# Performance work log

Hardware: AMD Instinct MI355X
Metric: run time of the kernel (lower is better)

The kernel has to match this reference:

```python
import jax, jax.numpy as jnp
import numpy as np
jax.config.update("jax_enable_x64", True)

MS_H = 10
MS_W = 10
EPS = 1e-8


def _window_mean(x, kh, kw):
    # x: [B, H, W]; VALID avg-pool with kernel (kh, kw), stride 1, via integral image
    c = jnp.cumsum(jnp.cumsum(x, axis=1), axis=2)
    c = jnp.pad(c, ((0, 0), (1, 0), (1, 0)))
    H, W = x.shape[1], x.shape[2]
    oh, ow = H - kh + 1, W - kw + 1
    s = (c[:, kh:kh + oh, kw:kw + ow] - c[:, :oh, kw:kw + ow]
         - c[:, kh:kh + oh, :ow] + c[:, :oh, :ow])
    return s / (kh * kw)


def _translate_bilinear(imgs, dy, dx):
    # imgs: [B, H, W]; out[b,i,j] = imgs[b, i - dy[b], j - dx[b]] (bilinear, zero fill)
    B, H, W = imgs.shape
    yq = jnp.arange(H, dtype=imgs.dtype)[None, :, None] - dy[:, None, None]
    xq = jnp.arange(W, dtype=imgs.dtype)[None, None, :] - dx[:, None, None]
    y0 = jnp.floor(yq); x0 = jnp.floor(xq)
    wy = yq - y0;       wx = xq - x0
    y0i = y0.astype(jnp.int32); x0i = x0.astype(jnp.int32)
    b = jnp.arange(B)[:, None, None]
    def samp(yi, xi):
        valid = (yi >= 0) & (yi < H) & (xi >= 0) & (xi < W)
        v = imgs[b, jnp.clip(yi, 0, H - 1), jnp.clip(xi, 0, W - 1)]
        return jnp.where(valid, v, jnp.zeros((), imgs.dtype))
    v00 = samp(y0i, x0i);     v01 = samp(y0i, x0i + 1)
    v10 = samp(y0i + 1, x0i); v11 = samp(y0i + 1, x0i + 1)
    return (v00 * (1 - wy) * (1 - wx) + v01 * (1 - wy) * wx
            + v10 * wy * (1 - wx) + v11 * wy * wx)


def _motion_correct(fr, template):
    # fr: [1, B, H, W, 1] float32; template: [H, W] float32
    B = fr.shape[1]
    H, W = template.shape
    mx, my = H // 2, W // 2
    # --- template normalization ---
    t_zm = template - jnp.mean(template)
    t_var = jnp.sum(jnp.square(t_zm)) + EPS
    target_freq = jnp.fft.fft2(t_zm.astype(jnp.complex128))            # [H, W]
    imgs = fr[0, :, :, :, 0]                                           # [B, H, W]
    imgs_zm = imgs - jnp.mean(imgs, axis=(1, 2), keepdims=True)
    # --- local statistics (avg_pool2d VALID, kernel = template minus shift margins) ---
    kh, kw = H - 2 * MS_W, W - 2 * MS_H
    m1 = _window_mean(imgs, kh, kw)                                    # [B, 2mw+1, 2mh+1]
    m2 = _window_mean(jnp.square(imgs), kh, kw)
    imgs_var = m2 - jnp.square(m1) / (kh * kw) + EPS
    imgs_var = jnp.where(imgs_var < 0, 0.0, imgs_var)
    denominator = jnp.sqrt(t_var * imgs_var)
    # --- FFT cross-correlation (fft3d over batch+spatial, exactly as the TF code) ---
    fr_freq = jnp.fft.fftn(imgs_zm.astype(jnp.complex128), axes=(0, 1, 2))
    img_product = fr_freq * jnp.conj(target_freq)[None]
    cc = jnp.abs(jnp.fft.ifftn(img_product, axes=(0, 1, 2))).astype(jnp.float32)
    rolled = jnp.roll(cc, (B, mx, my), axis=(0, 1, 2))
    nom = rolled[:, mx - MS_W:mx + MS_W + 1, my - MS_H:my + MS_H + 1]
    ncc = nom / denominator
    ncc = jnp.where(jnp.isnan(ncc), 0.0, ncc)                          # [B, 2mw+1, 2mh+1]
    # --- integer peak ---
    flat = ncc.reshape(B, -1)
    am = jnp.argmax(flat, axis=1)
    shx = am // (2 * MS_H + 1)
    shy = am % (2 * MS_H + 1)
    sh_x_n = -(shx - MS_H).astype(jnp.float32)
    sh_y_n = -(shy - MS_W).astype(jnp.float32)
    # --- log-parabolic sub-pixel refinement ---
    l = jnp.log(ncc)
    b = jnp.arange(B)
    lxm1 = l[b, shx - 1, shy]; lxp1 = l[b, shx + 1, shy]
    lym1 = l[b, shx, shy - 1]; lyp1 = l[b, shx, shy + 1]
    lc4 = 4.0 * l[b, shx, shy]
    sh_x_n = sh_x_n - (lxm1 - lxp1) / (2 * lxm1 - lc4 + 2 * lxp1)
    sh_y_n = sh_y_n - (lym1 - lyp1) / (2 * lym1 - lc4 + 2 * lyp1)
    # --- bilinear translate; tfa translations = [sh_y (dx, width), sh_x (dy, height)] ---
    warped = _translate_bilinear(imgs, sh_x_n, sh_y_n)                 # [B, H, W]
    return jnp.transpose(warped, (0, 2, 1)).reshape(B, H * W)


def setup_inputs() -> dict:
    H = W = 512
    B = 32
    k1, k2, k3 = jax.random.split(jax.random.key(0), 3)
    # smooth (low-pass) random template so the NCC peak is smooth/positive around its max
    noise = jax.random.normal(k1, (H, W))
    f = jnp.sqrt(jnp.fft.fftfreq(H)[:, None] ** 2 + jnp.fft.fftfreq(W)[None, :] ** 2)
    lp = (f < 0.05).astype(jnp.complex128)
    template = jnp.real(jnp.fft.ifft2(jnp.fft.fft2(noise) * lp))
    template = (template / template.std()).astype(jnp.float32)
    # frames: template shifted by small random integer offsets + noise
    shifts = jax.random.randint(k2, (B, 2), -5, 6)
    frames = jax.vmap(lambda s: jnp.roll(template, (s[0], s[1]), axis=(0, 1)))(shifts)
    frames = frames + 0.05 * jax.random.normal(k3, (B, H, W), dtype=jnp.float32)
    fr = frames[None, :, :, :, None].astype(jnp.float32)
    return {"fr": fr, "template": template}


def reference(fr, template):
    return _motion_correct(fr, template)
```

## Files before the change

kernel.cpp:

```cpp
#include <hip/hip_runtime.h>
#include <math.h>

#define HH 512
#define WW 512
#define NPIX (HH*WW)
#define NB 32
#define NS 21
#define KWIN 492
#define NKB 256
#define MT28 28
#define PARTSZ (MT28*32*16)
#define TPLB_COPY 278528

typedef __attribute__((ext_vector_type(8))) short short8;
typedef __attribute__((ext_vector_type(4))) float floatx4;

__device__ __forceinline__ unsigned short f2bf(float f) {
    unsigned u = __float_as_uint(f);
    unsigned r = (u + 0x7fffu + ((u >> 16) & 1u)) >> 16;
    return (unsigned short)r;
}

__device__ __forceinline__ short8 loadA(const unsigned short* p) {
    union { short8 v; unsigned u[4]; } r;
    const unsigned* q = (const unsigned*)p;
    r.u[0] = q[0]; r.u[1] = q[1]; r.u[2] = q[2]; r.u[3] = q[3];
    return r.v;
}

__global__ __launch_bounds__(512) void prep_tpl(
    const float* __restrict__ tpl, unsigned short* __restrict__ tplb)
{
    int t   = threadIdx.x;
    int sy0 = blockIdx.x * 4;
#pragma unroll
    for (int rr = 0; rr < 4; ++rr) {
        int sy = sy0 + rr;
        const float* srow = tpl + (size_t)sy * WW;
#pragma unroll
        for (int P = 0; P < 2; ++P) {
            for (int c = t; c < 544; c += 512) {
                int sx = (c + 496 - P) & 511;
                tplb[(size_t)P * TPLB_COPY + (size_t)sy * 544 + c] = f2bf(srow[sx]);
            }
        }
    }
}

__global__ __launch_bounds__(896) void corr_mfma(
    const float* __restrict__ fr, const unsigned short* __restrict__ tplb,
    const float* __restrict__ tpl, float* __restrict__ part,
    float* __restrict__ I1p, float* __restrict__ I2p,
    double* __restrict__ tplS1p, double* __restrict__ tplS2p)
{
    __shared__ unsigned short Bs[16384];
    __shared__ double jb1[8], jb2[8];

    const int blk = blockIdx.x;
    const int t   = threadIdx.x;

    if (blk >= 512) {
        int tj = blk - 512;
        if (t < 512) {
            const float* trow = tpl + (size_t)tj * 8 * WW;
            float s1 = 0.f, s2 = 0.f;
            for (int y = 0; y < 8; ++y) {
                float v = trow[(size_t)y * WW + t];
                s1 += v; s2 += v * v;
            }
            double d1 = (double)s1, d2 = (double)s2;
            for (int off = 32; off; off >>= 1) {
                d1 += __shfl_down(d1, off);
                d2 += __shfl_down(d2, off);
            }
            int lane = t & 63, wv = t >> 6;
            if (lane == 0) { jb1[wv] = d1; jb2[wv] = d2; }
        }
        __syncthreads();
        if (t == 0) {
            double a = 0.0, c = 0.0;
            for (int i = 0; i < 8; ++i) { a += jb1[i]; c += jb2[i]; }
            tplS1p[tj] = a; tplS2p[tj] = c;
        }
        return;
    }
    if (blk >= 256) {
        if (t < 512) {
            int id = blk - 256;
            int b = id >> 3, oct = id & 7;
            const float* img = fr + (size_t)b * NPIX;
            float s1 = 0.f, s2 = 0.f;
            int y0 = 20 + 59 * oct;
            for (int y = y0; y < y0 + 59; ++y) {
                float v = img[(size_t)y * WW + t];
                s1 += v; s2 += v * v;
            }
            I1p[(size_t)id * 512 + t] = s1;
            I2p[(size_t)id * 512 + t] = s2;
        }
        return;
    }

    const int l   = t & 63;
    const int wid = t >> 6;
    const int idx = blk;
    const int kb  = ((idx & 7) << 5) | (idx >> 3);
    const int kg  = l >> 4;
    const int ln  = l & 15;

    int du0, dv0, du1, dv1;
    {
        int m_g = 32 * wid + ln;
        du0 = (m_g * 1561) >> 15;
        dv0 = m_g - 21 * du0;
        if (m_g >= 441) { du0 = 0; dv0 = 0; }
        m_g = 32 * wid + 16 + ln;
        du1 = (m_g * 1561) >> 15;
        dv1 = m_g - 21 * du1;
        if (m_g >= 441) { du1 = 0; dv1 = 0; }
    }
    const int P0 = dv0 & 1, P1 = dv1 & 1;
    const int col0 = 8 * kg - dv0 + 26 + P0;
    const int col1 = 8 * kg - dv1 + 26 + P1;

    const unsigned short* lB = Bs + kg * 256 + ln * 8;

    floatx4 acc00 = {}, acc01 = {}, acc10 = {}, acc11 = {};

#pragma unroll 1
    for (int c = 0; c < 2; ++c) {
        const int row = 2 * kb + c;
        const int k0  = row << 9;
        if (c) __syncthreads();
        for (int i = t; i < 4096; i += 896) {
            int frame = i >> 7, q = i & 127;
            float4 v = *(const float4*)(fr + (size_t)frame * NPIX + k0 + 4 * q);
            int k8 = q >> 1, j4 = (q & 1) * 4;
            ushort4 o;
            o.x = f2bf(v.x); o.y = f2bf(v.y); o.z = f2bf(v.z); o.w = f2bf(v.w);
            *(ushort4*)&Bs[(k8 * 32 + frame) * 8 + j4] = o;
        }
        __syncthreads();

        const unsigned short* pA0 = tplb + (size_t)P0 * TPLB_COPY
            + (size_t)((row + 522 - du0) & 511) * 544 + col0;
        const unsigned short* pA1 = tplb + (size_t)P1 * TPLB_COPY
            + (size_t)((row + 522 - du1) & 511) * 544 + col1;

#pragma unroll
        for (int ks = 0; ks < 16; ++ks) {
            short8 A0 = loadA(pA0);
            short8 A1 = loadA(pA1);
            short8 B0 = *(const short8*)(lB + ks * 1024);
            short8 B1 = *(const short8*)(lB + ks * 1024 + 128);
            acc00 = __builtin_amdgcn_mfma_f32_16x16x32_bf16(A0, B0, acc00, 0, 0, 0);
            acc01 = __builtin_amdgcn_mfma_f32_16x16x32_bf16(A0, B1, acc01, 0, 0, 0);
            acc10 = __builtin_amdgcn_mfma_f32_16x16x32_bf16(A1, B0, acc10, 0, 0, 0);
            acc11 = __builtin_amdgcn_mfma_f32_16x16x32_bf16(A1, B1, acc11, 0, 0, 0);
            pA0 += 32; pA1 += 32;
        }
    }

    {
        size_t base = ((size_t)kb * MT28 + 2 * wid) * 32;
        floatx4* p;
        p = (floatx4*)(part + (base + ln)      * 16 + 4 * kg); *p = acc00;
        p = (floatx4*)(part + (base + 16 + ln) * 16 + 4 * kg); *p = acc01;
        p = (floatx4*)(part + (base + 32 + ln) * 16 + 4 * kg); *p = acc10;
        p = (floatx4*)(part + (base + 48 + ln) * 16 + 4 * kg); *p = acc11;
    }
}

__global__ __launch_bounds__(512) void reduce_k(
    const float* __restrict__ part, float* __restrict__ cc8)
{
    int blk = blockIdx.x;
    int oct = blk / 28;
    int j   = (blk % 28) * 512 + threadIdx.x;
    const float* p = part + (size_t)(oct * 32) * PARTSZ + j;
    float s = 0.f;
#pragma unroll 8
    for (int i = 0; i < 32; ++i)
        s += p[(size_t)i * PARTSZ];
    cc8[(size_t)oct * PARTSZ + j] = s;
}

__global__ __launch_bounds__(512) void stage2_am(
    const float* __restrict__ cc8, const float* __restrict__ fr,
    const float* __restrict__ I1p, const float* __restrict__ I2p,
    const double* __restrict__ tplS1p, const double* __restrict__ tplS2p,
    float* __restrict__ shifts)
{
    __shared__ double wr1[NS][8], wr2[NS][8], wrT[8];
    __shared__ float  e1[NS][40], e2[NS][40];
    __shared__ double totals1[NS], totals2[NS];
    __shared__ float  denomS[NS * NS];
    __shared__ double tS1s, tS2s, sum1b;

    int b = blockIdx.x;
    int x = threadIdx.x;
    const float* img = fr + (size_t)b * NPIX;
    float top[20], bot[20];
#pragma unroll
    for (int y = 0; y < 20; ++y) top[y] = img[(size_t)y * WW + x];
#pragma unroll
    for (int y = 0; y < 20; ++y) bot[y] = img[(size_t)(492 + y) * WW + x];

    float t1 = 0.f, t2 = 0.f, b1 = 0.f, b2 = 0.f;
#pragma unroll
    for (int y = 0; y < 20; ++y) {
        t1 += top[y]; t2 += top[y] * top[y];
        b1 += bot[y]; b2 += bot[y] * bot[y];
    }
    float i1 = 0.f, i2 = 0.f;
#pragma unroll
    for (int o = 0; o < 8; ++o) {
        i1 += I1p[((size_t)(b * 8 + o)) * 512 + x];
        i2 += I2p[((size_t)(b * 8 + o)) * 512 + x];
    }
    int lane = x & 63, wv = x >> 6;

    if (x < 64) {
        double d1 = tplS1p[x], d2 = tplS2p[x];
        for (int off = 32; off; off >>= 1) {
            d1 += __shfl_down(d1, off);
            d2 += __shfl_down(d2, off);
        }
        if (x == 0) { tS1s = d1; tS2s = d2; }
    }

    double tot = (double)i1 + (double)t1 + (double)b1;
    for (int off = 32; off; off >>= 1) tot += __shfl_down(tot, off);
    if (lane == 0) wrT[wv] = tot;

    float s1 = i1 + t1, s2 = i2 + t2;
#pragma unroll
    for (int u = 0; u < NS; ++u) {
        if (u) {
            float a = top[u-1], c = bot[u-1];
            s1 += c - a;
            s2 += c * c - a * a;
        }
        double d1 = (double)s1, d2 = (double)s2;
        for (int off = 32; off; off >>= 1) {
            d1 += __shfl_down(d1, off);
            d2 += __shfl_down(d2, off);
        }
        if (lane == 0) { wr1[u][wv] = d1; wr2[u][wv] = d2; }
        if (x < 20)        { e1[u][x]       = s1; e2[u][x]       = s2; }
        else if (x >= 492) { e1[u][x - 472] = s1; e2[u][x - 472] = s2; }
    }
    __syncthreads();
    if (x == 0) {
        double s = 0.0;
        for (int i = 0; i < 8; ++i) s += wrT[i];
        sum1b = s;
    }
    if (x < NS) {
        double a = 0.0, c = 0.0;
        for (int i = 0; i < 8; ++i) { a += wr1[x][i]; c += wr2[x][i]; }
        totals1[x] = a; totals2[x] = c;
    }
    __syncthreads();
    if (x < NS * NS) {
        int u = x / NS, v = x - NS * u;
        double S1 = totals1[u], S2 = totals2[u];
        for (int j = 0; j < v; ++j)  { S1 -= (double)e1[u][j];      S2 -= (double)e2[u][j]; }
        for (int j = v; j < 20; ++j) { S1 -= (double)e1[u][20 + j]; S2 -= (double)e2[u][20 + j]; }
        const double inv = 1.0 / ((double)KWIN * (double)KWIN);
        double m1 = S1 * inv, m2 = S2 * inv;
        double var = m2 - (m1 * m1) * inv + 1e-8;
        if (var < 0.0) var = 0.0;
        double tv = tS2s - tS1s * tS1s * (1.0 / (double)NPIX) + 1e-8;
        denomS[x] = (float)sqrt(tv * var);
    }
    __syncthreads();

    if (x < 64) {
        float corr = (float)(sum1b * tS1s * (1.0 / (double)NPIX));
        auto ccAt = [&](int m) -> float {
            int jj = ((m >> 4) * 512) + b * 16 + (m & 15);
            float s = 0.f;
#pragma unroll
            for (int o = 0; o < 8; ++o) s += cc8[(size_t)o * PARTSZ + jj];
            return s;
        };
        float best = -1e30f; int bidx = NS * NS;
        for (int i = x; i < NS * NS; i += 64) {
            float v = fabsf(ccAt(i) - corr) / denomS[i];
            if (v != v) v = 0.f;
            if (v > best) { best = v; bidx = i; }
        }
        for (int off = 32; off; off >>= 1) {
            float ov = __shfl_down(best, off);
            int   oi = __shfl_down(bidx, off);
            if (ov > best || (ov == best && oi < bidx)) { best = ov; bidx = oi; }
        }
        if (x == 0) {
            int shx = bidx / NS, shy = bidx % NS;
            auto nccAt = [&](int i, int j) -> float {
                i = (i < 0) ? i + NS : i; i = (i > NS - 1) ? NS - 1 : i;
                j = (j < 0) ? j + NS : j; j = (j > NS - 1) ? NS - 1 : j;
                float v = fabsf(ccAt(i * NS + j) - corr) / denomS[i * NS + j];
                if (v != v) v = 0.f;
                return v;
            };
            float lc  = logf(nccAt(shx, shy));
            float lxm = logf(nccAt(shx - 1, shy));
            float lxp = logf(nccAt(shx + 1, shy));
            float lym = logf(nccAt(shx, shy - 1));
            float lyp = logf(nccAt(shx, shy + 1));
            float shxn = -(float)(shx - 10) - (lxm - lxp) / (2.f * lxm - 4.f * lc + 2.f * lxp);
            float shyn = -(float)(shy - 10) - (lym - lyp) / (2.f * lym - 4.f * lc + 2.f * lyp);
            shifts[b]      = shxn;
            shifts[32 + b] = shyn;
        }
    }
}

__device__ __forceinline__ float samp(const float* __restrict__ img, int y, int x) {
    bool valid = (y >= 0) & (y < HH) & (x >= 0) & (x < WW);
    int yc = min(max(y, 0), HH - 1), xc = min(max(x, 0), WW - 1);
    float v = img[(size_t)yc * WW + xc];
    return valid ? v : 0.f;
}

__global__ __launch_bounds__(256) void warp_kernel(
    const float* __restrict__ fr, const float* __restrict__ shifts,
    float* __restrict__ out)
{
    int b  = blockIdx.z;
    int h0 = blockIdx.y * 32;
    int w0 = blockIdx.x * 32;
    float dy = shifts[b], dx = shifts[32 + b];
    const float* img = fr + (size_t)b * NPIX;
    __shared__ float tile[32][33];
    int tx = threadIdx.x & 31;
    int tz = threadIdx.x >> 5;
#pragma unroll
    for (int s = 0; s < 4; ++s) {
        int h = h0 + tz + 8 * s;
        int w = w0 + tx;
        float yq = (float)h - dy;
        float xq = (float)w - dx;
        float y0f = floorf(yq), x0f = floorf(xq);
        float wy = yq - y0f, wx = xq - x0f;
        int y0 = (int)y0f, x0 = (int)x0f;
        float v00 = samp(img, y0,     x0);
        float v01 = samp(img, y0,     x0 + 1);
        float v10 = samp(img, y0 + 1, x0);
        float v11 = samp(img, y0 + 1, x0 + 1);
        float val = v00 * (1.f - wy) * (1.f - wx) + v01 * (1.f - wy) * wx
                  + v10 * wy * (1.f - wx)         + v11 * wy * wx;
        tile[tz + 8 * s][tx] = val;
    }
    __syncthreads();
#pragma unroll
    for (int s = 0; s < 4; ++s) {
        int hh = tx;
        int ww = tz + 8 * s;
        out[(size_t)b * NPIX + (size_t)(w0 + ww) * HH + (h0 + hh)] = tile[hh][ww];
    }
}

extern "C" void kernel_launch(void* const* d_in, const int* in_sizes, int n_in,
                              void* d_out, int out_size, void* d_ws, size_t ws_size,
                              hipStream_t stream) {
    const float* fr  = (const float*)d_in[0];
    const float* tpl = (const float*)d_in[1];
    float* out = (float*)d_out;
    char* ws = (char*)d_ws;

    unsigned short* tplb = (unsigned short*)(ws + 0);
    float*  I1p    = (float*) (ws + 2097152);
    float*  I2p    = (float*) (ws + 2621440);
    double* tplS1p = (double*)(ws + 3145728);
    double* tplS2p = (double*)(ws + 3146240);
    float*  shifts = (float*) (ws + 3146752);
    float*  cc8    = (float*) (ws + 4194304);
    float*  part   = (float*) (ws + 8388608);

    prep_tpl  <<<128, 512, 0, stream>>>(tpl, tplb);
    corr_mfma <<<576, 896, 0, stream>>>(fr, tplb, tpl, part, I1p, I2p, tplS1p, tplS2p);
    reduce_k  <<<224, 512, 0, stream>>>(part, cc8);
    stage2_am <<<32, 512, 0, stream>>>(cc8, fr, I1p, I2p, tplS1p, tplS2p, shifts);
    warp_kernel<<<dim3(16, 16, 32), 256, 0, stream>>>(fr, shifts, out);
}
```

Baseline: 147.3 us.

## Precompute border row sums in corr kernel and simplify stage2 window totals

Adds 160 extra blocks to the correlation kernel that compute per-row double sums and sums of squares for the 20 top and 20 bottom rows of each frame. Stage2 then builds the 21 row-shift window totals with a serial prefix update instead of 21 block-wide shuffle reductions. Only the edge columns still load the bottom rows to fill the per-column edge tables. The intent is to shorten the serial, single-block-per-frame stage2 kernel. The cost is extra blocks in corr_mfma, and the window totals now mix double row sums with float column accumulations, which changes rounding slightly.

New measurement: 136.1 us. 1.08x faster.

```diff
diff --git a/kernel.cpp b/kernel.cpp
--- a/kernel.cpp
+++ b/kernel.cpp
@@ -51,7 +51,8 @@
     const float* __restrict__ fr, const unsigned short* __restrict__ tplb,
     const float* __restrict__ tpl, float* __restrict__ part,
     float* __restrict__ I1p, float* __restrict__ I2p,
-    double* __restrict__ tplS1p, double* __restrict__ tplS2p)
+    double* __restrict__ tplS1p, double* __restrict__ tplS2p,
+    double* __restrict__ rowS1, double* __restrict__ rowS2)
 {
     __shared__ unsigned short Bs[16384];
     __shared__ double jb1[8], jb2[8];
@@ -59,6 +60,29 @@
     const int blk = blockIdx.x;
     const int t   = threadIdx.x;
 
+    if (blk >= 576) {
+        int wvv = t >> 6;
+        if (wvv < 8) {
+            int rid  = (blk - 576) * 8 + wvv;
+            int lane = t & 63;
+            int b = rid / 40, j2 = rid % 40;
+            int y = (j2 < 20) ? j2 : (472 + j2);
+            const float* row = fr + (size_t)b * NPIX + (size_t)y * WW;
+            double d1 = 0.0, d2 = 0.0;
+#pragma unroll
+            for (int i = 0; i < 8; ++i) {
+                float v = row[lane + 64 * i];
+                d1 += (double)v;
+                d2 += (double)(v * v);
+            }
+            for (int off = 32; off; off >>= 1) {
+                d1 += __shfl_down(d1, off);
+                d2 += __shfl_down(d2, off);
+            }
+            if (lane == 0) { rowS1[rid] = d1; rowS2[rid] = d2; }
+        }
+        return;
+    }
     if (blk >= 512) {
         int tj = blk - 512;
         if (t < 512) {
@@ -189,29 +213,27 @@
     const float* __restrict__ cc8, const float* __restrict__ fr,
     const float* __restrict__ I1p, const float* __restrict__ I2p,
     const double* __restrict__ tplS1p, const double* __restrict__ tplS2p,
+    const double* __restrict__ rowS1, const double* __restrict__ rowS2,
     float* __restrict__ shifts)
 {
-    __shared__ double wr1[NS][8], wr2[NS][8], wrT[8];
     __shared__ float  e1[NS][40], e2[NS][40];
     __shared__ double totals1[NS], totals2[NS];
     __shared__ float  denomS[NS * NS];
     __shared__ double tS1s, tS2s, sum1b;
+    __shared__ double w1[8], w2[8];
+    __shared__ double rs1[40], rs2[40];
 
     int b = blockIdx.x;
     int x = threadIdx.x;
     const float* img = fr + (size_t)b * NPIX;
-    float top[20], bot[20];
+
+    float top[20];
 #pragma unroll
     for (int y = 0; y < 20; ++y) top[y] = img[(size_t)y * WW + x];
-#pragma unroll
-    for (int y = 0; y < 20; ++y) bot[y] = img[(size_t)(492 + y) * WW + x];
-
-    float t1 = 0.f, t2 = 0.f, b1 = 0.f, b2 = 0.f;
-#pragma unroll
-    for (int y = 0; y < 20; ++y) {
-        t1 += top[y]; t2 += top[y] * top[y];
-        b1 += bot[y]; b2 += bot[y] * bot[y];
-    }
+    float t1 = 0.f, t2 = 0.f;
+#pragma unroll
+    for (int y = 0; y < 20; ++y) { t1 += top[y]; t2 += top[y] * top[y]; }
+
     float i1 = 0.f, i2 = 0.f;
 #pragma unroll
     for (int o = 0; o < 8; ++o) {
@@ -219,6 +241,8 @@
         i2 += I2p[((size_t)(b * 8 + o)) * 512 + x];
     }
     int lane = x & 63, wv = x >> 6;
+
+    if (x < 40) { rs1[x] = rowS1[b * 40 + x]; rs2[x] = rowS2[b * 40 + x]; }
 
     if (x < 64) {
         double d1 = tplS1p[x], d2 = tplS2p[x];
@@ -229,39 +253,49 @@
         if (x == 0) { tS1s = d1; tS2s = d2; }
     }
 
-    double tot = (double)i1 + (double)t1 + (double)b1;
-    for (int off = 32; off; off >>= 1) tot += __shfl_down(tot, off);
-    if (lane == 0) wrT[wv] = tot;
-
-    float s1 = i1 + t1, s2 = i2 + t2;
-#pragma unroll
-    for (int u = 0; u < NS; ++u) {
-        if (u) {
-            float a = top[u-1], c = bot[u-1];
-            s1 += c - a;
-            s2 += c * c - a * a;
-        }
-        double d1 = (double)s1, d2 = (double)s2;
+    {
+        double d1 = (double)(i1 + t1), d2 = (double)(i2 + t2);
         for (int off = 32; off; off >>= 1) {
             d1 += __shfl_down(d1, off);
             d2 += __shfl_down(d2, off);
         }
-        if (lane == 0) { wr1[u][wv] = d1; wr2[u][wv] = d2; }
-        if (x < 20)        { e1[u][x]       = s1; e2[u][x]       = s2; }
-        else if (x >= 492) { e1[u][x - 472] = s1; e2[u][x - 472] = s2; }
+        if (lane == 0) { w1[wv] = d1; w2[wv] = d2; }
+    }
+
+    if (x < 20 || x >= 492) {
+        float bot[20];
+#pragma unroll
+        for (int y = 0; y < 20; ++y) bot[y] = img[(size_t)(492 + y) * WW + x];
+        int xi = (x < 20) ? x : (x - 472);
+        float s1 = i1 + t1, s2 = i2 + t2;
+#pragma unroll
+        for (int u = 0; u < NS; ++u) {
+            if (u) {
+                float a = top[u-1], c = bot[u-1];
+                s1 += c - a;
+                s2 += c * c - a * a;
+            }
+            e1[u][xi] = s1; e2[u][xi] = s2;
+        }
     }
     __syncthreads();
+
     if (x == 0) {
-        double s = 0.0;
-        for (int i = 0; i < 8; ++i) s += wrT[i];
-        sum1b = s;
-    }
-    if (x < NS) {
         double a = 0.0, c = 0.0;
-        for (int i = 0; i < 8; ++i) { a += wr1[x][i]; c += wr2[x][i]; }
-        totals1[x] = a; totals2[x] = c;
+        for (int i = 0; i < 8; ++i) { a += w1[i]; c += w2[i]; }
+        double p1 = a, p2 = c;
+        totals1[0] = p1; totals2[0] = p2;
+        for (int u = 1; u < NS; ++u) {
+            p1 += rs1[20 + u - 1] - rs1[u - 1];
+            p2 += rs2[20 + u - 1] - rs2[u - 1];
+            totals1[u] = p1; totals2[u] = p2;
+        }
+        double sb = 0.0;
+        for (int j = 0; j < 20; ++j) sb += rs1[20 + j];
+        sum1b = a + sb;
     }
     __syncthreads();
+
     if (x < NS * NS) {
         int u = x / NS, v = x - NS * u;
         double S1 = totals1[u], S2 = totals2[u];
@@ -377,12 +411,16 @@
     double* tplS1p = (double*)(ws + 3145728);
     double* tplS2p = (double*)(ws + 3146240);
     float*  shifts = (float*) (ws + 3146752);
+    double* rowS1  = (double*)(ws + 3276800);
+    double* rowS2  = (double*)(ws + 3287040);
     float*  cc8    = (float*) (ws + 4194304);
     float*  part   = (float*) (ws + 8388608);
 
     prep_tpl  <<<128, 512, 0, stream>>>(tpl, tplb);
-    corr_mfma <<<576, 896, 0, stream>>>(fr, tplb, tpl, part, I1p, I2p, tplS1p, tplS2p);
+    corr_mfma <<<736, 896, 0, stream>>>(fr, tplb, tpl, part, I1p, I2p,
+                                        tplS1p, tplS2p, rowS1, rowS2);
     reduce_k  <<<224, 512, 0, stream>>>(part, cc8);
-    stage2_am <<<32, 512, 0, stream>>>(cc8, fr, I1p, I2p, tplS1p, tplS2p, shifts);
+    stage2_am <<<32, 512, 0, stream>>>(cc8, fr, I1p, I2p, tplS1p, tplS2p,
+                                       rowS1, rowS2, shifts);
     warp_kernel<<<dim3(16, 16, 32), 256, 0, stream>>>(fr, shifts, out);
 }
```
